# Kernel optimization log

Hardware: AMD Instinct MI355X
Metric: run time of the kernel (lower is better)

Reference implementation:

```python
import jax, jax.numpy as jnp
import numpy as np

B, PAST, FUT, D = 128, 256, 128, 128
RU, LD, FC, TL = 512, 128, 512, 128
HDEC = RU + LD  # 640


def _u(k, shape, s):
    return jax.random.uniform(k, shape, jnp.float32, -s, s)


def setup_inputs() -> dict:
    key = jax.random.key(0)
    ks = jax.random.split(key, 40)
    s_ru = 1.0 / np.sqrt(RU)
    s_hd = 1.0 / np.sqrt(HDEC)
    inp = {
        "past": jax.random.normal(ks[0], (B, PAST, D), jnp.float32),
        "future": jax.random.normal(ks[1], (B, FUT, D), jnp.float32),
        "eps": jax.random.normal(ks[2], (B, LD), jnp.float32),
        # encoder GRU over past (rnn_phi)
        "phi_Wih": _u(ks[3], (3 * RU, D), s_ru), "phi_Whh": _u(ks[4], (3 * RU, RU), s_ru),
        "phi_bih": _u(ks[5], (3 * RU,), s_ru), "phi_bhh": _u(ks[6], (3 * RU,), s_ru),
        # encoder GRU over future (rnn_x)
        "xr_Wih": _u(ks[7], (3 * RU, D), s_ru), "xr_Whh": _u(ks[8], (3 * RU, RU), s_ru),
        "xr_bih": _u(ks[9], (3 * RU,), s_ru), "xr_bhh": _u(ks[10], (3 * RU,), s_ru),
        # encoder_mu MLP: 2*RU -> 512 -> 256 -> LD
        "mu_W1": _u(ks[11], (512, 2 * RU), 1 / np.sqrt(2 * RU)), "mu_b1": _u(ks[12], (512,), 1 / np.sqrt(2 * RU)),
        "mu_W2": _u(ks[13], (256, 512), 1 / np.sqrt(512)), "mu_b2": _u(ks[14], (256,), 1 / np.sqrt(512)),
        "mu_W3": _u(ks[15], (LD, 256), 1 / np.sqrt(256)), "mu_b3": _u(ks[16], (LD,), 1 / np.sqrt(256)),
        # encoder_logvar MLP
        "lv_W1": _u(ks[17], (512, 2 * RU), 1 / np.sqrt(2 * RU)), "lv_b1": _u(ks[18], (512,), 1 / np.sqrt(2 * RU)),
        "lv_W2": _u(ks[19], (256, 512), 1 / np.sqrt(512)), "lv_b2": _u(ks[20], (256,), 1 / np.sqrt(512)),
        "lv_W3": _u(ks[21], (LD, 256), 1 / np.sqrt(256)), "lv_b3": _u(ks[22], (LD,), 1 / np.sqrt(256)),
        # decoder GRU: input D -> hidden HDEC
        "dec_Wih": _u(ks[23], (3 * HDEC, D), s_hd), "dec_Whh": _u(ks[24], (3 * HDEC, HDEC), s_hd),
        "dec_bih": _u(ks[25], (3 * HDEC,), s_hd), "dec_bhh": _u(ks[26], (3 * HDEC,), s_hd),
        # decoder heads
        "fc_W": _u(ks[27], (FC, HDEC), s_hd), "fc_b": _u(ks[28], (FC,), s_hd),
        "out_W": _u(ks[29], (D, FC), 1 / np.sqrt(FC)), "out_b": _u(ks[30], (D,), 1 / np.sqrt(FC)),
    }
    return inp


def _gru_cell(x, h, Wih, Whh, bih, bhh):
    # torch GRU cell math
    gi = x @ Wih.T + bih
    gh = h @ Whh.T + bhh
    ir, iz, inn = jnp.split(gi, 3, axis=-1)
    hr, hz, hn = jnp.split(gh, 3, axis=-1)
    r = jax.nn.sigmoid(ir + hr)
    z = jax.nn.sigmoid(iz + hz)
    n = jnp.tanh(inn + r * hn)
    return (1.0 - z) * n + z * h


def _gru_final_hidden(x, Wih, Whh, bih, bhh):
    # x: [B, T, D] -> final hidden [B, H]
    h0 = jnp.zeros((x.shape[0], Whh.shape[1]), x.dtype)
    def step(h, xt):
        h = _gru_cell(xt, h, Wih, Whh, bih, bhh)
        return h, None
    hT, _ = jax.lax.scan(step, h0, jnp.swapaxes(x, 0, 1))
    return hT


def _mlp(f, W1, b1, W2, b2, W3, b3):
    h = jax.nn.leaky_relu(f @ W1.T + b1)
    h = jax.nn.leaky_relu(h @ W2.T + b2)
    return h @ W3.T + b3


def _forward(past, future, eps,
             phi_Wih, phi_Whh, phi_bih, phi_bhh,
             xr_Wih, xr_Whh, xr_bih, xr_bhh,
             mu_W1, mu_b1, mu_W2, mu_b2, mu_W3, mu_b3,
             lv_W1, lv_b1, lv_W2, lv_b2, lv_W3, lv_b3,
             dec_Wih, dec_Whh, dec_bih, dec_bhh,
             fc_W, fc_b, out_W, out_b):
    # encoder
    h_past = _gru_final_hidden(past, phi_Wih, phi_Whh, phi_bih, phi_bhh)      # [B, RU]
    h_future = _gru_final_hidden(future, xr_Wih, xr_Whh, xr_bih, xr_bhh)      # [B, RU]
    features = jnp.concatenate([h_past, h_future], axis=1)                    # [B, 2*RU]
    z_mu = _mlp(features, mu_W1, mu_b1, mu_W2, mu_b2, mu_W3, mu_b3)
    z_logvar = _mlp(features, lv_W1, lv_b1, lv_W2, lv_b2, lv_W3, lv_b3)
    # reparameterize
    z = z_mu + eps * jnp.exp(0.5 * z_logvar)                                  # [B, LD]
    dec_h0 = jnp.concatenate([h_past, z], axis=1)                             # [B, HDEC]
    x0 = past[:, -1, :]                                                       # [B, D]
    def step(carry, _):
        x_in, h = carry
        h = _gru_cell(x_in, h, dec_Wih, dec_Whh, dec_bih, dec_bhh)
        out = jax.nn.relu(h @ fc_W.T + fc_b) @ out_W.T + out_b                # [B, D]
        return (out, h), out
    _, outs = jax.lax.scan(step, (x0, dec_h0), None, length=TL)               # [TL, B, D]
    x_mu = jnp.swapaxes(outs, 0, 1)                                           # [B, TL, D]
    return x_mu, z_mu, z_logvar


def reference(past, future, eps,
              phi_Wih, phi_Whh, phi_bih, phi_bhh,
              xr_Wih, xr_Whh, xr_bih, xr_bhh,
              mu_W1, mu_b1, mu_W2, mu_b2, mu_W3, mu_b3,
              lv_W1, lv_b1, lv_W2, lv_b2, lv_W3, lv_b3,
              dec_Wih, dec_Whh, dec_bih, dec_bhh,
              fc_W, fc_b, out_W, out_b):
    return _forward(past, future, eps,
                    phi_Wih, phi_Whh, phi_bih, phi_bhh,
                    xr_Wih, xr_Whh, xr_bih, xr_bhh,
                    mu_W1, mu_b1, mu_W2, mu_b2, mu_W3, mu_b3,
                    lv_W1, lv_b1, lv_W2, lv_b2, lv_W3, lv_b3,
                    dec_Wih, dec_Whh, dec_bih, dec_bhh,
                    fc_W, fc_b, out_W, out_b)
```

## Files before the change

### kernel.cpp

```cpp
#include <hip/hip_runtime.h>
#include <math.h>

constexpr int B    = 128;
constexpr int PAST = 256;
constexpr int FUT  = 128;
constexpr int D    = 128;
constexpr int RU   = 512;
constexpr int LD   = 128;
constexpr int TL   = 128;
constexpr int HDEC = 640;

typedef __bf16 bf16x8 __attribute__((ext_vector_type(8)));
typedef float  f32x4  __attribute__((ext_vector_type(4)));
typedef unsigned short u16x8 __attribute__((ext_vector_type(8)));

__device__ __forceinline__ unsigned short f2bf(float f) {
    unsigned int x = __float_as_uint(f);
    x = (x + 0x7fffu + ((x >> 16) & 1u)) >> 16;
    return (unsigned short)x;
}
__device__ __forceinline__ float bf2f(unsigned short u) {
    return __uint_as_float(((unsigned int)u) << 16);
}
__device__ __forceinline__ float sigm_(float x) { return 1.f / (1.f + __expf(-x)); }
__device__ __forceinline__ float tanh_(float x) {
    float e = __expf(2.f * x);
    return 1.f - 2.f / (e + 1.f);
}
__device__ __forceinline__ bf16x8 ldsfrag(const unsigned short* p) {
    return *reinterpret_cast<const bf16x8*>(p);
}
__device__ __forceinline__ f32x4 mfma16(bf16x8 a, bf16x8 b, f32x4 c) {
    return __builtin_amdgcn_mfma_f32_16x16x32_bf16(a, b, c, 0, 0, 0);
}

__global__ __launch_bounds__(256) void split_plain(
    const float* __restrict__ W, unsigned short* __restrict__ hi,
    unsigned short* __restrict__ lo, int n)
{
    for (int i = blockIdx.x * 256 + threadIdx.x; i < n; i += gridDim.x * 256) {
        float v = W[i];
        unsigned short h = f2bf(v);
        hi[i] = h;
        lo[i] = f2bf(v - bf2f(h));
    }
}

__global__ __launch_bounds__(256) void split_pack(
    const float* __restrict__ Wih, const float* __restrict__ Whh,
    int DXc, int Hc, int N3,
    unsigned short* __restrict__ hi, unsigned short* __restrict__ lo)
{
    int K = DXc + Hc;
    int total = N3 * K;
    for (int i = blockIdx.x * 256 + threadIdx.x; i < total; i += gridDim.x * 256) {
        int n = i / K, k = i - n * K;
        float v = (k < DXc) ? Wih[(size_t)n * DXc + k]
                            : Whh[(size_t)n * Hc + (k - DXc)];
        unsigned short h = f2bf(v);
        hi[i] = h;
        lo[i] = f2bf(v - bf2f(h));
    }
}

struct StepArgs {
    const float* x;  int sx;
    const float* h_in;
    const unsigned short* Whi;
    const unsigned short* Wlo;
    const float* bih; const float* bhh;
    float* h_out;
};

template<int NSET>
__device__ __forceinline__ void step_compute(
    const unsigned short* sA0, const unsigned short* sA1,
    const unsigned short* sW0, const unsigned short* sW1,
    int nlocal, int arow, int koff, f32x4 (&acc)[4][4])
{
    constexpr int LDR = 40;
    bf16x8 wh[3], wl[3];
    #pragma unroll
    for (int g = 0; g < 3; ++g) {
        wh[g] = ldsfrag(&sW0[(g * 64 + nlocal) * LDR + koff]);
        wl[g] = ldsfrag(&sW1[(g * 64 + nlocal) * LDR + koff]);
    }
    #pragma unroll
    for (int mf = 0; mf < 4; ++mf) {
        bf16x8 ah = ldsfrag(&sA0[(mf * 16 + arow) * LDR + koff]);
        bf16x8 al = ldsfrag(&sA1[(mf * 16 + arow) * LDR + koff]);
        acc[mf][0] = mfma16(ah, wh[0], acc[mf][0]);
        acc[mf][0] = mfma16(ah, wl[0], acc[mf][0]);
        acc[mf][0] = mfma16(al, wh[0], acc[mf][0]);
        acc[mf][1] = mfma16(ah, wh[1], acc[mf][1]);
        acc[mf][1] = mfma16(ah, wl[1], acc[mf][1]);
        acc[mf][1] = mfma16(al, wh[1], acc[mf][1]);
        acc[mf][NSET] = mfma16(ah, wh[2], acc[mf][NSET]);
        acc[mf][NSET] = mfma16(ah, wl[2], acc[mf][NSET]);
        acc[mf][NSET] = mfma16(al, wh[2], acc[mf][NSET]);
    }
}

template<int H, int DX>
__global__ __launch_bounds__(256, 1) void gru_step_mfma(StepArgs A0, StepArgs A1)
{
    constexpr int K   = DX + H;
    constexpr int NC  = K / 32;
    constexpr int XC  = DX / 32;
    constexpr int LDR = 40;

    __shared__ unsigned short sA[2][64 * LDR];
    __shared__ unsigned short sW[2][3 * 64 * LDR];

    const StepArgs A = (blockIdx.z == 0) ? A0 : A1;
    const int m0   = blockIdx.x * 64;
    const int hc0  = blockIdx.y * 64;
    const int tid  = threadIdx.x;
    const int lane = tid & 63;
    const int w    = tid >> 6;
    const int arow = lane & 15;
    const int koff = (lane >> 4) * 8;
    const int nlocal = w * 16 + arow;

    f32x4 acc[4][4];
    #pragma unroll
    for (int i = 0; i < 4; ++i)
        #pragma unroll
        for (int j = 0; j < 4; ++j) acc[i][j] = f32x4{0.f, 0.f, 0.f, 0.f};

    float4 ar[2];
    u16x8  wreg[6];

    auto load_chunk = [&](int c) {
        const int k0 = c * 32;
        #pragma unroll
        for (int j = 0; j < 2; ++j) {
            int id = tid + j * 256;
            int row = id >> 3, c4 = id & 7;
            const float* src = (k0 < DX)
                ? (A.x + (size_t)(m0 + row) * A.sx + (k0 + c4 * 4))
                : (A.h_in + (size_t)(m0 + row) * H + (k0 - DX + c4 * 4));
            ar[j] = *reinterpret_cast<const float4*>(src);
        }
        #pragma unroll
        for (int j = 0; j < 6; ++j) {
            int id = tid + j * 256;
            int half = (id >= 768) ? 1 : 0;
            int rem = id - half * 768;
            int gate = rem >> 8;
            int rr = (rem >> 2) & 63;
            int c8 = rem & 3;
            const unsigned short* Wp = half ? A.Wlo : A.Whi;
            wreg[j] = *reinterpret_cast<const u16x8*>(
                Wp + (size_t)(gate * H + hc0 + rr) * K + k0 + c8 * 8);
        }
    };

    auto write_chunk = [&]() {
        #pragma unroll
        for (int j = 0; j < 2; ++j) {
            int id = tid + j * 256;
            int row = id >> 3, c4 = id & 7;
            float v[4] = {ar[j].x, ar[j].y, ar[j].z, ar[j].w};
            unsigned short hs[4], ls[4];
            #pragma unroll
            for (int q = 0; q < 4; ++q) {
                hs[q] = f2bf(v[q]);
                ls[q] = f2bf(v[q] - bf2f(hs[q]));
            }
            uint2 hp, lp;
            hp.x = (unsigned)hs[0] | ((unsigned)hs[1] << 16);
            hp.y = (unsigned)hs[2] | ((unsigned)hs[3] << 16);
            lp.x = (unsigned)ls[0] | ((unsigned)ls[1] << 16);
            lp.y = (unsigned)ls[2] | ((unsigned)ls[3] << 16);
            *reinterpret_cast<uint2*>(&sA[0][row * LDR + c4 * 4]) = hp;
            *reinterpret_cast<uint2*>(&sA[1][row * LDR + c4 * 4]) = lp;
        }
        #pragma unroll
        for (int j = 0; j < 6; ++j) {
            int id = tid + j * 256;
            int half = (id >= 768) ? 1 : 0;
            int rem = id - half * 768;
            int gate = rem >> 8;
            int rr = (rem >> 2) & 63;
            int c8 = rem & 3;
            *reinterpret_cast<u16x8*>(&sW[half][(gate * 64 + rr) * LDR + c8 * 8]) = wreg[j];
        }
    };

    load_chunk(0);
    write_chunk();
    __syncthreads();
    for (int c = 0; c < NC; ++c) {
        if (c + 1 < NC) load_chunk(c + 1);
        if (c < XC) step_compute<2>(sA[0], sA[1], sW[0], sW[1], nlocal, arow, koff, acc);
        else        step_compute<3>(sA[0], sA[1], sW[0], sW[1], nlocal, arow, koff, acc);
        __syncthreads();
        if (c + 1 < NC) { write_chunk(); __syncthreads(); }
    }

    const int hc = hc0 + nlocal;
    const float bir = A.bih[hc],         bhr = A.bhh[hc];
    const float biz = A.bih[H + hc],     bhz = A.bhh[H + hc];
    const float bin = A.bih[2 * H + hc], bhn = A.bhh[2 * H + hc];
    #pragma unroll
    for (int mf = 0; mf < 4; ++mf) {
        #pragma unroll
        for (int r = 0; r < 4; ++r) {
            int m = m0 + mf * 16 + (lane >> 4) * 4 + r;
            float rg = sigm_(acc[mf][0][r] + bir + bhr);
            float zg = sigm_(acc[mf][1][r] + biz + bhz);
            float ng = tanh_((acc[mf][2][r] + bin) + rg * (acc[mf][3][r] + bhn));
            float ho = A.h_in[(size_t)m * H + hc];
            A.h_out[(size_t)m * H + hc] = (1.f - zg) * ng + zg * ho;
        }
    }
}

__global__ __launch_bounds__(256, 1) void gemm_mfma(
    const float* __restrict__ A, int lda,
    const unsigned short* __restrict__ Whi, const unsigned short* __restrict__ Wlo,
    int K, const float* __restrict__ bias,
    float* __restrict__ C, int ldc, int act)
{
    constexpr int LDR = 72;
    __shared__ unsigned short sA[2][64 * LDR];
    __shared__ unsigned short sW[2][128 * LDR];

    const int m0 = blockIdx.x * 64;
    const int n0 = blockIdx.y * 128;
    const int tid = threadIdx.x;
    const int lane = tid & 63;
    const int w = tid >> 6;
    const int arow = lane & 15;
    const int koff = (lane >> 4) * 8;

    f32x4 acc[4][2];
    #pragma unroll
    for (int i = 0; i < 4; ++i) { acc[i][0] = f32x4{0,0,0,0}; acc[i][1] = f32x4{0,0,0,0}; }

    float4 ar[4];
    u16x8  wreg[8];
    const int NC = K / 64;

    auto load_chunk = [&](int c) {
        const int k0 = c * 64;
        #pragma unroll
        for (int j = 0; j < 4; ++j) {
            int id = tid + j * 256;
            int row = id >> 4, c4 = id & 15;
            ar[j] = *reinterpret_cast<const float4*>(A + (size_t)(m0 + row) * lda + k0 + c4 * 4);
        }
        #pragma unroll
        for (int j = 0; j < 8; ++j) {
            int id = tid + j * 256;
            int half = id >> 10;
            int rem = id & 1023;
            int row = rem >> 3, c8 = rem & 7;
            const unsigned short* Wp = half ? Wlo : Whi;
            wreg[j] = *reinterpret_cast<const u16x8*>(
                Wp + (size_t)(n0 + row) * K + k0 + c8 * 8);
        }
    };
    auto write_chunk = [&]() {
        #pragma unroll
        for (int j = 0; j < 4; ++j) {
            int id = tid + j * 256;
            int row = id >> 4, c4 = id & 15;
            float v[4] = {ar[j].x, ar[j].y, ar[j].z, ar[j].w};
            unsigned short hs[4], ls[4];
            #pragma unroll
            for (int q = 0; q < 4; ++q) {
                hs[q] = f2bf(v[q]);
                ls[q] = f2bf(v[q] - bf2f(hs[q]));
            }
            uint2 hp, lp;
            hp.x = (unsigned)hs[0] | ((unsigned)hs[1] << 16);
            hp.y = (unsigned)hs[2] | ((unsigned)hs[3] << 16);
            lp.x = (unsigned)ls[0] | ((unsigned)ls[1] << 16);
            lp.y = (unsigned)ls[2] | ((unsigned)ls[3] << 16);
            *reinterpret_cast<uint2*>(&sA[0][row * LDR + c4 * 4]) = hp;
            *reinterpret_cast<uint2*>(&sA[1][row * LDR + c4 * 4]) = lp;
        }
        #pragma unroll
        for (int j = 0; j < 8; ++j) {
            int id = tid + j * 256;
            int half = id >> 10;
            int rem = id & 1023;
            int row = rem >> 3, c8 = rem & 7;
            *reinterpret_cast<u16x8*>(&sW[half][row * LDR + c8 * 8]) = wreg[j];
        }
    };

    load_chunk(0);
    write_chunk();
    __syncthreads();
    for (int c = 0; c < NC; ++c) {
        if (c + 1 < NC) load_chunk(c + 1);
        #pragma unroll
        for (int ks = 0; ks < 2; ++ks) {
            bf16x8 wh[2], wl[2];
            #pragma unroll
            for (int nf = 0; nf < 2; ++nf) {
                wh[nf] = ldsfrag(&sW[0][(w * 32 + nf * 16 + arow) * LDR + ks * 32 + koff]);
                wl[nf] = ldsfrag(&sW[1][(w * 32 + nf * 16 + arow) * LDR + ks * 32 + koff]);
            }
            #pragma unroll
            for (int mf = 0; mf < 4; ++mf) {
                bf16x8 ah = ldsfrag(&sA[0][(mf * 16 + arow) * LDR + ks * 32 + koff]);
                bf16x8 al = ldsfrag(&sA[1][(mf * 16 + arow) * LDR + ks * 32 + koff]);
                #pragma unroll
                for (int nf = 0; nf < 2; ++nf) {
                    acc[mf][nf] = mfma16(ah, wh[nf], acc[mf][nf]);
                    acc[mf][nf] = mfma16(ah, wl[nf], acc[mf][nf]);
                    acc[mf][nf] = mfma16(al, wh[nf], acc[mf][nf]);
                }
            }
        }
        __syncthreads();
        if (c + 1 < NC) { write_chunk(); __syncthreads(); }
    }

    #pragma unroll
    for (int mf = 0; mf < 4; ++mf) {
        #pragma unroll
        for (int nf = 0; nf < 2; ++nf) {
            int n = n0 + w * 32 + nf * 16 + arow;
            float bv = bias[n];
            #pragma unroll
            for (int r = 0; r < 4; ++r) {
                int m = m0 + mf * 16 + (lane >> 4) * 4 + r;
                float v = acc[mf][nf][r] + bv;
                if (act == 1)      v = (v > 0.f) ? v : 0.01f * v;
                else if (act == 2) v = fmaxf(v, 0.f);
                C[(size_t)m * ldc + n] = v;
            }
        }
    }
}

__global__ __launch_bounds__(256) void concat2(
    const float* __restrict__ A, int ka,
    const float* __restrict__ Bp, int kb,
    float* __restrict__ Y, int M)
{
    int wdt = ka + kb;
    int idx = blockIdx.x * 256 + threadIdx.x;
    if (idx >= M * wdt) return;
    int m = idx / wdt, c = idx - m * wdt;
    Y[idx] = (c < ka) ? A[(size_t)m * ka + c] : Bp[(size_t)m * kb + (c - ka)];
}

__global__ __launch_bounds__(256) void reparam(
    const float* __restrict__ zmu, const float* __restrict__ zlv,
    const float* __restrict__ eps, float* __restrict__ z, int n)
{
    int i = blockIdx.x * 256 + threadIdx.x;
    if (i < n) z[i] = zmu[i] + eps[i] * __expf(0.5f * zlv[i]);
}

extern "C" void kernel_launch(void* const* d_in, const int* in_sizes, int n_in,
                              void* d_out, int out_size, void* d_ws, size_t ws_size,
                              hipStream_t stream)
{
    const float* past    = (const float*)d_in[0];
    const float* future  = (const float*)d_in[1];
    const float* eps     = (const float*)d_in[2];
    const float* phi_Wih = (const float*)d_in[3];
    const float* phi_Whh = (const float*)d_in[4];
    const float* phi_bih = (const float*)d_in[5];
    const float* phi_bhh = (const float*)d_in[6];
    const float* xr_Wih  = (const float*)d_in[7];
    const float* xr_Whh  = (const float*)d_in[8];
    const float* xr_bih  = (const float*)d_in[9];
    const float* xr_bhh  = (const float*)d_in[10];
    const float* mu_W1   = (const float*)d_in[11];
    const float* mu_b1   = (const float*)d_in[12];
    const float* mu_W2   = (const float*)d_in[13];
    const float* mu_b2   = (const float*)d_in[14];
    const float* mu_W3   = (const float*)d_in[15];
    const float* mu_b3   = (const float*)d_in[16];
    const float* lv_W1   = (const float*)d_in[17];
    const float* lv_b1   = (const float*)d_in[18];
    const float* lv_W2   = (const float*)d_in[19];
    const float* lv_b2   = (const float*)d_in[20];
    const float* lv_W3   = (const float*)d_in[21];
    const float* lv_b3   = (const float*)d_in[22];
    const float* dec_Wih = (const float*)d_in[23];
    const float* dec_Whh = (const float*)d_in[24];
    const float* dec_bih = (const float*)d_in[25];
    const float* dec_bhh = (const float*)d_in[26];
    const float* fc_W    = (const float*)d_in[27];
    const float* fc_b    = (const float*)d_in[28];
    const float* out_W   = (const float*)d_in[29];
    const float* out_b   = (const float*)d_in[30];
    (void)in_sizes; (void)n_in; (void)out_size; (void)ws_size;

    float* out = (float*)d_out;
    float* xmu = out;
    float* zmu = out + (size_t)B * TL * D;
    float* zlv = zmu + (size_t)B * LD;

    char* p = (char*)d_ws;
    auto aus = [&](size_t n) { unsigned short* r = (unsigned short*)p; p += ((n * 2 + 255) / 256) * 256; return r; };
    auto af  = [&](size_t n) { float* r = (float*)p; p += ((n * 4 + 255) / 256) * 256; return r; };

    unsigned short* phiWhi = aus((size_t)3 * RU * (D + RU));
    unsigned short* phiWlo = aus((size_t)3 * RU * (D + RU));
    unsigned short* xrWhi  = aus((size_t)3 * RU * (D + RU));
    unsigned short* xrWlo  = aus((size_t)3 * RU * (D + RU));
    unsigned short* decWhi = aus((size_t)3 * HDEC * (D + HDEC));
    unsigned short* decWlo = aus((size_t)3 * HDEC * (D + HDEC));
    unsigned short* mW1hi = aus(512 * 1024), *mW1lo = aus(512 * 1024);
    unsigned short* mW2hi = aus(256 * 512),  *mW2lo = aus(256 * 512);
    unsigned short* mW3hi = aus(128 * 256),  *mW3lo = aus(128 * 256);
    unsigned short* lW1hi = aus(512 * 1024), *lW1lo = aus(512 * 1024);
    unsigned short* lW2hi = aus(256 * 512),  *lW2lo = aus(256 * 512);
    unsigned short* lW3hi = aus(128 * 256),  *lW3lo = aus(128 * 256);
    unsigned short* fcWhi = aus(512 * 640),  *fcWlo = aus(512 * 640);
    unsigned short* oWhi  = aus(128 * 512),  *oWlo  = aus(128 * 512);

    float* hA  = af((size_t)B * RU);
    float* hB  = af((size_t)B * RU);
    float* hxA = af((size_t)B * RU);
    float* hxB = af((size_t)B * RU);
    float* dA  = af((size_t)B * HDEC);
    float* dB  = af((size_t)B * HDEC);
    float* feat= af((size_t)B * 2 * RU);
    float* m1  = af((size_t)B * 512);
    float* m2  = af((size_t)B * 256);
    float* zb  = af((size_t)B * LD);
    float* fcb = af((size_t)B * 512);

    dim3 blk(256);

    split_pack<<<512, blk, 0, stream>>>(phi_Wih, phi_Whh, D, RU, 3 * RU, phiWhi, phiWlo);
    split_pack<<<512, blk, 0, stream>>>(xr_Wih,  xr_Whh,  D, RU, 3 * RU, xrWhi,  xrWlo);
    split_pack<<<512, blk, 0, stream>>>(dec_Wih, dec_Whh, D, HDEC, 3 * HDEC, decWhi, decWlo);
    split_plain<<<512, blk, 0, stream>>>(mu_W1, mW1hi, mW1lo, 512 * 1024);
    split_plain<<<256, blk, 0, stream>>>(mu_W2, mW2hi, mW2lo, 256 * 512);
    split_plain<<<128, blk, 0, stream>>>(mu_W3, mW3hi, mW3lo, 128 * 256);
    split_plain<<<512, blk, 0, stream>>>(lv_W1, lW1hi, lW1lo, 512 * 1024);
    split_plain<<<256, blk, 0, stream>>>(lv_W2, lW2hi, lW2lo, 256 * 512);
    split_plain<<<128, blk, 0, stream>>>(lv_W3, lW3hi, lW3lo, 128 * 256);
    split_plain<<<512, blk, 0, stream>>>(fc_W, fcWhi, fcWlo, 512 * 640);
    split_plain<<<128, blk, 0, stream>>>(out_W, oWhi, oWlo, 128 * 512);

    hipMemsetAsync(hA,  0, (size_t)B * RU * sizeof(float), stream);
    hipMemsetAsync(hxA, 0, (size_t)B * RU * sizeof(float), stream);

    for (int t = 0; t < PAST; ++t) {
        const float* phin  = (t & 1) ? hB : hA;
        float*       phout = (t & 1) ? hA : hB;
        StepArgs pa{past + (size_t)t * D, PAST * D, phin, phiWhi, phiWlo, phi_bih, phi_bhh, phout};
        if (t < FUT) {
            const float* xin  = (t & 1) ? hxB : hxA;
            float*       xout = (t & 1) ? hxA : hxB;
            StepArgs xa{future + (size_t)t * D, FUT * D, xin, xrWhi, xrWlo, xr_bih, xr_bhh, xout};
            gru_step_mfma<RU, D><<<dim3(2, RU / 64, 2), blk, 0, stream>>>(pa, xa);
        } else {
            gru_step_mfma<RU, D><<<dim3(2, RU / 64, 1), blk, 0, stream>>>(pa, pa);
        }
    }

    concat2<<<dim3((B * 2 * RU + 255) / 256), blk, 0, stream>>>(hA, RU, hxA, RU, feat, B);

    gemm_mfma<<<dim3(2, 4), blk, 0, stream>>>(feat, 2 * RU, mW1hi, mW1lo, 1024, mu_b1, m1, 512, 1);
    gemm_mfma<<<dim3(2, 2), blk, 0, stream>>>(m1, 512, mW2hi, mW2lo, 512, mu_b2, m2, 256, 1);
    gemm_mfma<<<dim3(2, 1), blk, 0, stream>>>(m2, 256, mW3hi, mW3lo, 256, mu_b3, zmu, LD, 0);
    gemm_mfma<<<dim3(2, 4), blk, 0, stream>>>(feat, 2 * RU, lW1hi, lW1lo, 1024, lv_b1, m1, 512, 1);
    gemm_mfma<<<dim3(2, 2), blk, 0, stream>>>(m1, 512, lW2hi, lW2lo, 512, lv_b2, m2, 256, 1);
    gemm_mfma<<<dim3(2, 1), blk, 0, stream>>>(m2, 256, lW3hi, lW3lo, 256, lv_b3, zlv, LD, 0);

    reparam<<<dim3((B * LD + 255) / 256), blk, 0, stream>>>(zmu, zlv, eps, zb, B * LD);
    concat2<<<dim3((B * HDEC + 255) / 256), blk, 0, stream>>>(hA, RU, zb, LD, dA, B);

    for (int t = 0; t < TL; ++t) {
        const float* xin; int sx;
        if (t == 0) { xin = past + (size_t)(PAST - 1) * D; sx = PAST * D; }
        else        { xin = xmu + (size_t)(t - 1) * D;     sx = TL * D; }
        const float* hin  = (t & 1) ? dB : dA;
        float*       hout = (t & 1) ? dA : dB;
        StepArgs da{xin, sx, hin, decWhi, decWlo, dec_bih, dec_bhh, hout};
        gru_step_mfma<HDEC, D><<<dim3(2, HDEC / 64, 1), blk, 0, stream>>>(da, da);
        gemm_mfma<<<dim3(2, 4), blk, 0, stream>>>(hout, HDEC, fcWhi, fcWlo, HDEC, fc_b, fcb, 512, 2);
        gemm_mfma<<<dim3(2, 1), blk, 0, stream>>>(fcb, 512, oWhi, oWlo, 512, out_b, xmu + (size_t)t * D, TL * D, 0);
    }
}
```

Measured before the change: 15.03 ms.

## Replace per-timestep GRU launches with persistent kernels using grid barriers

The encoder and decoder recurrences now each run as one persistent kernel rather than one launch per timestep. Workgroups keep their slice of the hi-part bf16 weights resident in LDS across all timesteps and synchronise between steps with an atomic-counter grid barrier. In the decoder, the GRU, the fc layer and the output layer run as roles inside the same kernel, separated by barriers. This removes hundreds of launch gaps and repeated weight reloads. In exchange it relies on every workgroup being co-resident (128 or 80 WGs), which is not guaranteed, and the spin barriers add latency on every step.

```diff
diff --git a/kernel.cpp b/kernel.cpp
--- a/kernel.cpp
+++ b/kernel.cpp
@@ -32,6 +32,28 @@
 }
 __device__ __forceinline__ f32x4 mfma16(bf16x8 a, bf16x8 b, f32x4 c) {
     return __builtin_amdgcn_mfma_f32_16x16x32_bf16(a, b, c, 0, 0, 0);
+}
+__device__ __forceinline__ void cvt4(const float4& v, uint2& hp, uint2& lp) {
+    float a[4] = {v.x, v.y, v.z, v.w};
+    unsigned short hs[4], ls[4];
+    #pragma unroll
+    for (int q = 0; q < 4; ++q) { hs[q] = f2bf(a[q]); ls[q] = f2bf(a[q] - bf2f(hs[q])); }
+    hp.x = (unsigned)hs[0] | ((unsigned)hs[1] << 16);
+    hp.y = (unsigned)hs[2] | ((unsigned)hs[3] << 16);
+    lp.x = (unsigned)ls[0] | ((unsigned)ls[1] << 16);
+    lp.y = (unsigned)ls[2] | ((unsigned)ls[3] << 16);
+}
+
+__device__ __forceinline__ void coop_barrier(unsigned* cnt, unsigned nwg, unsigned rnd) {
+    __syncthreads();
+    __threadfence();
+    if (threadIdx.x == 0) {
+        __hip_atomic_fetch_add(cnt, 1u, __ATOMIC_RELEASE, __HIP_MEMORY_SCOPE_AGENT);
+        unsigned tgt = (rnd + 1u) * nwg;
+        while (__hip_atomic_load(cnt, __ATOMIC_ACQUIRE, __HIP_MEMORY_SCOPE_AGENT) < tgt)
+            __builtin_amdgcn_s_sleep(2);
+    }
+    __syncthreads();
 }
 
 __global__ __launch_bounds__(256) void split_plain(
@@ -63,157 +85,364 @@
     }
 }
 
-struct StepArgs {
-    const float* x;  int sx;
-    const float* h_in;
-    const unsigned short* Whi;
-    const unsigned short* Wlo;
+struct EncArgs {
+    const float* x; int xstride; int T;
+    const unsigned short* Whi; const unsigned short* Wlo;
     const float* bih; const float* bhh;
-    float* h_out;
+    float* h0; float* h1;
+    unsigned* bar;
 };
 
-template<int NSET>
-__device__ __forceinline__ void step_compute(
-    const unsigned short* sA0, const unsigned short* sA1,
-    const unsigned short* sW0, const unsigned short* sW1,
-    int nlocal, int arow, int koff, f32x4 (&acc)[4][4])
-{
-    constexpr int LDR = 40;
-    bf16x8 wh[3], wl[3];
-    #pragma unroll
-    for (int g = 0; g < 3; ++g) {
-        wh[g] = ldsfrag(&sW0[(g * 64 + nlocal) * LDR + koff]);
-        wl[g] = ldsfrag(&sW1[(g * 64 + nlocal) * LDR + koff]);
-    }
-    #pragma unroll
-    for (int mf = 0; mf < 4; ++mf) {
-        bf16x8 ah = ldsfrag(&sA0[(mf * 16 + arow) * LDR + koff]);
-        bf16x8 al = ldsfrag(&sA1[(mf * 16 + arow) * LDR + koff]);
-        acc[mf][0] = mfma16(ah, wh[0], acc[mf][0]);
-        acc[mf][0] = mfma16(ah, wl[0], acc[mf][0]);
-        acc[mf][0] = mfma16(al, wh[0], acc[mf][0]);
-        acc[mf][1] = mfma16(ah, wh[1], acc[mf][1]);
-        acc[mf][1] = mfma16(ah, wl[1], acc[mf][1]);
-        acc[mf][1] = mfma16(al, wh[1], acc[mf][1]);
-        acc[mf][NSET] = mfma16(ah, wh[2], acc[mf][NSET]);
-        acc[mf][NSET] = mfma16(ah, wl[2], acc[mf][NSET]);
-        acc[mf][NSET] = mfma16(al, wh[2], acc[mf][NSET]);
-    }
-}
-
-template<int H, int DX>
-__global__ __launch_bounds__(256, 1) void gru_step_mfma(StepArgs A0, StepArgs A1)
-{
-    constexpr int K   = DX + H;
-    constexpr int NC  = K / 32;
-    constexpr int XC  = DX / 32;
-    constexpr int LDR = 40;
-
-    __shared__ unsigned short sA[2][64 * LDR];
-    __shared__ unsigned short sW[2][3 * 64 * LDR];
-
-    const StepArgs A = (blockIdx.z == 0) ? A0 : A1;
-    const int m0   = blockIdx.x * 64;
-    const int hc0  = blockIdx.y * 64;
-    const int tid  = threadIdx.x;
+__global__ __launch_bounds__(256, 1) void enc_kernel(EncArgs P, EncArgs X)
+{
+    constexpr int H = 512, DX = 128, K = 640, NCH = 20, XC = 4, LDK = 648, SR = 40;
+    __shared__ unsigned short sWhi[48 * LDK];
+    __shared__ unsigned short sAh[2][64 * SR];
+    __shared__ unsigned short sAl[2][64 * SR];
+    __shared__ unsigned short sWl[2][48 * SR];
+
+    const int wg = blockIdx.x;
+    const EncArgs A = (wg < 64) ? P : X;
+    const int lwg = wg & 63;
+    const int m0  = (lwg & 1) * 64;
+    const int c0  = (lwg >> 1) * 16;
+    const int tid = threadIdx.x;
     const int lane = tid & 63;
-    const int w    = tid >> 6;
+    const int w = tid >> 6;
     const int arow = lane & 15;
     const int koff = (lane >> 4) * 8;
-    const int nlocal = w * 16 + arow;
-
-    f32x4 acc[4][4];
+
+    for (int i = tid; i < 48 * 80; i += 256) {
+        int rr = i / 80, c8 = i % 80;
+        int g = rr >> 4, j = rr & 15;
+        *reinterpret_cast<u16x8*>(&sWhi[rr * LDK + c8 * 8]) =
+            *reinterpret_cast<const u16x8*>(A.Whi + (size_t)(g * H + c0 + j) * K + c8 * 8);
+    }
+    const unsigned short* wloB = nullptr;
+    if (tid < 192) {
+        int rr = tid >> 2, c8 = tid & 3;
+        int g = rr >> 4, j = rr & 15;
+        wloB = A.Wlo + (size_t)(g * H + c0 + j) * K + c8 * 8;
+    }
+    const int hc = c0 + arow;
+    const float brz0 = A.bih[hc] + A.bhh[hc];
+    const float brz1 = A.bih[H + hc] + A.bhh[H + hc];
+    const float bn_i = A.bih[2 * H + hc];
+    const float bn_h = A.bhh[2 * H + hc];
+    __syncthreads();
+
+    float4 ar[2]; u16x8 wl;
+
+    for (int t = 0; t < A.T; ++t) {
+        const float* hin  = (t & 1) ? A.h1 : A.h0;
+        float*       hout = (t & 1) ? A.h0 : A.h1;
+        const float* xp = A.x + (size_t)t * D;
+
+        f32x4 accR = {0,0,0,0}, accZ = {0,0,0,0}, accNx = {0,0,0,0}, accNh = {0,0,0,0};
+
+        auto ldc = [&](int c) {
+            int k0 = c * 32;
+            #pragma unroll
+            for (int j = 0; j < 2; ++j) {
+                int id = tid + j * 256;
+                int row = id >> 3, c4 = id & 7;
+                const float* src = (k0 < DX)
+                    ? (xp + (size_t)(m0 + row) * A.xstride + k0 + c4 * 4)
+                    : (hin + (size_t)(m0 + row) * H + (k0 - DX) + c4 * 4);
+                ar[j] = *reinterpret_cast<const float4*>(src);
+            }
+            if (wloB) wl = *reinterpret_cast<const u16x8*>(wloB + k0);
+        };
+        auto wrc = [&](int b) {
+            #pragma unroll
+            for (int j = 0; j < 2; ++j) {
+                int id = tid + j * 256;
+                int row = id >> 3, c4 = id & 7;
+                uint2 hp, lp; cvt4(ar[j], hp, lp);
+                *reinterpret_cast<uint2*>(&sAh[b][row * SR + c4 * 4]) = hp;
+                *reinterpret_cast<uint2*>(&sAl[b][row * SR + c4 * 4]) = lp;
+            }
+            if (wloB) {
+                int rr = tid >> 2, c8 = tid & 3;
+                *reinterpret_cast<u16x8*>(&sWl[b][rr * SR + c8 * 8]) = wl;
+            }
+        };
+
+        ldc(0); wrc(0); __syncthreads();
+        for (int c = 0; c < NCH; ++c) {
+            const int b = c & 1;
+            if (c + 1 < NCH) ldc(c + 1);
+            const int aoff = (w * 16 + arow) * SR + koff;
+            bf16x8 ah = ldsfrag(&sAh[b][aoff]);
+            bf16x8 al = ldsfrag(&sAl[b][aoff]);
+            bf16x8 whR = ldsfrag(&sWhi[(arow) * LDK + c * 32 + koff]);
+            bf16x8 whZ = ldsfrag(&sWhi[(16 + arow) * LDK + c * 32 + koff]);
+            bf16x8 whN = ldsfrag(&sWhi[(32 + arow) * LDK + c * 32 + koff]);
+            bf16x8 wlR = ldsfrag(&sWl[b][(arow) * SR + koff]);
+            bf16x8 wlZ = ldsfrag(&sWl[b][(16 + arow) * SR + koff]);
+            bf16x8 wlN = ldsfrag(&sWl[b][(32 + arow) * SR + koff]);
+            accR = mfma16(ah, whR, accR); accR = mfma16(ah, wlR, accR); accR = mfma16(al, whR, accR);
+            accZ = mfma16(ah, whZ, accZ); accZ = mfma16(ah, wlZ, accZ); accZ = mfma16(al, whZ, accZ);
+            if (c < XC) {
+                accNx = mfma16(ah, whN, accNx); accNx = mfma16(ah, wlN, accNx); accNx = mfma16(al, whN, accNx);
+            } else {
+                accNh = mfma16(ah, whN, accNh); accNh = mfma16(ah, wlN, accNh); accNh = mfma16(al, whN, accNh);
+            }
+            if (c + 1 < NCH) wrc(b ^ 1);
+            __syncthreads();
+        }
+
+        #pragma unroll
+        for (int r = 0; r < 4; ++r) {
+            int m = m0 + w * 16 + (lane >> 4) * 4 + r;
+            float rg = sigm_(accR[r] + brz0);
+            float zg = sigm_(accZ[r] + brz1);
+            float ng = tanh_((accNx[r] + bn_i) + rg * (accNh[r] + bn_h));
+            float ho = hin[(size_t)m * H + hc];
+            hout[(size_t)m * H + hc] = (1.f - zg) * ng + zg * ho;
+        }
+        coop_barrier(A.bar, 64, (unsigned)t);
+    }
+}
+
+struct DecArgs {
+    const float* past_last;
+    float* xmu;
+    const unsigned short* Whi; const unsigned short* Wlo;
+    const float* bih; const float* bhh;
+    const unsigned short* fcWhi; const unsigned short* fcWlo;
+    const float* fc_b;
+    const unsigned short* oWhi; const unsigned short* oWlo;
+    const float* out_b;
+    float* dh0; float* dh1; float* fcb;
+    unsigned* bar;
+};
+
+__device__ __forceinline__ void plain16(
+    unsigned short* smem, int whi_ush, int ldk, int nch,
+    const float* src, int srcld,
+    const unsigned short* wloB,
+    float bias_v, int mode,
+    float* dst, long dld, int dcol0,
+    int tid, int w, int lane, int arow, int koff)
+{
+    unsigned short* AH[2] = { smem + whi_ush,          smem + whi_ush + 5120 };
+    unsigned short* AL[2] = { smem + whi_ush + 10240,  smem + whi_ush + 15360 };
+    unsigned short* WL[2] = { smem + whi_ush + 20480,  smem + whi_ush + 21120 };
+    f32x4 acc0 = {0,0,0,0}, acc1 = {0,0,0,0};
+    float4 ar[4]; u16x8 wl;
+    auto ldc = [&](int c) {
+        int k0 = c * 32;
+        #pragma unroll
+        for (int j = 0; j < 4; ++j) {
+            int id = tid + j * 256, row = id >> 3, c4 = id & 7;
+            ar[j] = *reinterpret_cast<const float4*>(src + (size_t)row * srcld + k0 + c4 * 4);
+        }
+        if (wloB) wl = *reinterpret_cast<const u16x8*>(wloB + k0);
+    };
+    auto wrc = [&](int b) {
+        #pragma unroll
+        for (int j = 0; j < 4; ++j) {
+            int id = tid + j * 256, row = id >> 3, c4 = id & 7;
+            uint2 hp, lp; cvt4(ar[j], hp, lp);
+            *reinterpret_cast<uint2*>(&AH[b][row * 40 + c4 * 4]) = hp;
+            *reinterpret_cast<uint2*>(&AL[b][row * 40 + c4 * 4]) = lp;
+        }
+        if (wloB) {
+            int rr = tid >> 2, c8 = tid & 3;
+            *reinterpret_cast<u16x8*>(&WL[b][rr * 40 + c8 * 8]) = wl;
+        }
+    };
+    ldc(0); wrc(0); __syncthreads();
+    for (int c = 0; c < nch; ++c) {
+        int b = c & 1;
+        if (c + 1 < nch) ldc(c + 1);
+        int a0 = (w * 32 + arow) * 40 + koff;
+        bf16x8 ah0 = ldsfrag(&AH[b][a0]),       al0 = ldsfrag(&AL[b][a0]);
+        bf16x8 ah1 = ldsfrag(&AH[b][a0 + 640]), al1 = ldsfrag(&AL[b][a0 + 640]);
+        bf16x8 wh  = ldsfrag(&smem[arow * ldk + c * 32 + koff]);
+        bf16x8 wlg = ldsfrag(&WL[b][arow * 40 + koff]);
+        acc0 = mfma16(ah0, wh, acc0); acc0 = mfma16(ah0, wlg, acc0); acc0 = mfma16(al0, wh, acc0);
+        acc1 = mfma16(ah1, wh, acc1); acc1 = mfma16(ah1, wlg, acc1); acc1 = mfma16(al1, wh, acc1);
+        if (c + 1 < nch) wrc(b ^ 1);
+        __syncthreads();
+    }
     #pragma unroll
-    for (int i = 0; i < 4; ++i)
-        #pragma unroll
-        for (int j = 0; j < 4; ++j) acc[i][j] = f32x4{0.f, 0.f, 0.f, 0.f};
-
-    float4 ar[2];
-    u16x8  wreg[6];
-
-    auto load_chunk = [&](int c) {
-        const int k0 = c * 32;
-        #pragma unroll
-        for (int j = 0; j < 2; ++j) {
-            int id = tid + j * 256;
-            int row = id >> 3, c4 = id & 7;
-            const float* src = (k0 < DX)
-                ? (A.x + (size_t)(m0 + row) * A.sx + (k0 + c4 * 4))
-                : (A.h_in + (size_t)(m0 + row) * H + (k0 - DX + c4 * 4));
-            ar[j] = *reinterpret_cast<const float4*>(src);
-        }
-        #pragma unroll
-        for (int j = 0; j < 6; ++j) {
-            int id = tid + j * 256;
-            int half = (id >= 768) ? 1 : 0;
-            int rem = id - half * 768;
-            int gate = rem >> 8;
-            int rr = (rem >> 2) & 63;
-            int c8 = rem & 3;
-            const unsigned short* Wp = half ? A.Wlo : A.Whi;
-            wreg[j] = *reinterpret_cast<const u16x8*>(
-                Wp + (size_t)(gate * H + hc0 + rr) * K + k0 + c8 * 8);
-        }
+    for (int mf = 0; mf < 2; ++mf) {
+        f32x4 a = mf ? acc1 : acc0;
+        #pragma unroll
+        for (int r = 0; r < 4; ++r) {
+            int m = w * 32 + mf * 16 + (lane >> 4) * 4 + r;
+            float v = a[r] + bias_v;
+            if (mode == 1) v = fmaxf(v, 0.f);
+            dst[(size_t)m * dld + dcol0 + arow] = v;
+        }
+    }
+}
+
+__device__ __forceinline__ void dec_gru(
+    unsigned short* smem, const DecArgs& A, int t,
+    const float* hcur, float* hnext,
+    int c0, const unsigned short* wloB,
+    float brz0, float brz1, float bn_i, float bn_h,
+    int tid, int w, int lane, int arow, int koff)
+{
+    unsigned short* AH[2] = { smem + 37248, smem + 42368 };
+    unsigned short* AL[2] = { smem + 47488, smem + 52608 };
+    unsigned short* WL[2] = { smem + 57728, smem + 59648 };
+    const float* xp; long xs;
+    if (t == 0) { xp = A.past_last; xs = (long)PAST * D; }
+    else        { xp = A.xmu + (size_t)(t - 1) * D; xs = (long)TL * D; }
+
+    f32x4 aR0 = {0,0,0,0}, aZ0 = aR0, aNx0 = aR0, aNh0 = aR0;
+    f32x4 aR1 = aR0, aZ1 = aR0, aNx1 = aR0, aNh1 = aR0;
+    float4 ar[4]; u16x8 wl;
+    auto ldc = [&](int c) {
+        int k0 = c * 32;
+        #pragma unroll
+        for (int j = 0; j < 4; ++j) {
+            int id = tid + j * 256, row = id >> 3, c4 = id & 7;
+            const float* s = (k0 < D)
+                ? (xp + (size_t)row * xs + k0 + c4 * 4)
+                : (hcur + (size_t)row * HDEC + (k0 - D) + c4 * 4);
+            ar[j] = *reinterpret_cast<const float4*>(s);
+        }
+        if (wloB) wl = *reinterpret_cast<const u16x8*>(wloB + k0);
     };
-
-    auto write_chunk = [&]() {
-        #pragma unroll
-        for (int j = 0; j < 2; ++j) {
-            int id = tid + j * 256;
-            int row = id >> 3, c4 = id & 7;
-            float v[4] = {ar[j].x, ar[j].y, ar[j].z, ar[j].w};
-            unsigned short hs[4], ls[4];
-            #pragma unroll
-            for (int q = 0; q < 4; ++q) {
-                hs[q] = f2bf(v[q]);
-                ls[q] = f2bf(v[q] - bf2f(hs[q]));
-            }
-            uint2 hp, lp;
-            hp.x = (unsigned)hs[0] | ((unsigned)hs[1] << 16);
-            hp.y = (unsigned)hs[2] | ((unsigned)hs[3] << 16);
-            lp.x = (unsigned)ls[0] | ((unsigned)ls[1] << 16);
-            lp.y = (unsigned)ls[2] | ((unsigned)ls[3] << 16);
-            *reinterpret_cast<uint2*>(&sA[0][row * LDR + c4 * 4]) = hp;
-            *reinterpret_cast<uint2*>(&sA[1][row * LDR + c4 * 4]) = lp;
-        }
-        #pragma unroll
-        for (int j = 0; j < 6; ++j) {
-            int id = tid + j * 256;
-            int half = (id >= 768) ? 1 : 0;
-            int rem = id - half * 768;
-            int gate = rem >> 8;
-            int rr = (rem >> 2) & 63;
-            int c8 = rem & 3;
-            *reinterpret_cast<u16x8*>(&sW[half][(gate * 64 + rr) * LDR + c8 * 8]) = wreg[j];
+    auto wrc = [&](int b) {
+        #pragma unroll
+        for (int j = 0; j < 4; ++j) {
+            int id = tid + j * 256, row = id >> 3, c4 = id & 7;
+            uint2 hp, lp; cvt4(ar[j], hp, lp);
+            *reinterpret_cast<uint2*>(&AH[b][row * 40 + c4 * 4]) = hp;
+            *reinterpret_cast<uint2*>(&AL[b][row * 40 + c4 * 4]) = lp;
+        }
+        if (wloB) {
+            int rr = tid >> 2, c8 = tid & 3;
+            *reinterpret_cast<u16x8*>(&WL[b][rr * 40 + c8 * 8]) = wl;
         }
     };
-
-    load_chunk(0);
-    write_chunk();
+    ldc(0); wrc(0); __syncthreads();
+    for (int c = 0; c < 24; ++c) {
+        int b = c & 1;
+        if (c + 1 < 24) ldc(c + 1);
+        int a0 = (w * 32 + arow) * 40 + koff;
+        bf16x8 ah0 = ldsfrag(&AH[b][a0]),       al0 = ldsfrag(&AL[b][a0]);
+        bf16x8 ah1 = ldsfrag(&AH[b][a0 + 640]), al1 = ldsfrag(&AL[b][a0 + 640]);
+        bf16x8 whR = ldsfrag(&smem[(arow) * 776 + c * 32 + koff]);
+        bf16x8 whZ = ldsfrag(&smem[(16 + arow) * 776 + c * 32 + koff]);
+        bf16x8 whN = ldsfrag(&smem[(32 + arow) * 776 + c * 32 + koff]);
+        bf16x8 wlR = ldsfrag(&WL[b][(arow) * 40 + koff]);
+        bf16x8 wlZ = ldsfrag(&WL[b][(16 + arow) * 40 + koff]);
+        bf16x8 wlN = ldsfrag(&WL[b][(32 + arow) * 40 + koff]);
+        aR0 = mfma16(ah0, whR, aR0); aR0 = mfma16(ah0, wlR, aR0); aR0 = mfma16(al0, whR, aR0);
+        aR1 = mfma16(ah1, whR, aR1); aR1 = mfma16(ah1, wlR, aR1); aR1 = mfma16(al1, whR, aR1);
+        aZ0 = mfma16(ah0, whZ, aZ0); aZ0 = mfma16(ah0, wlZ, aZ0); aZ0 = mfma16(al0, whZ, aZ0);
+        aZ1 = mfma16(ah1, whZ, aZ1); aZ1 = mfma16(ah1, wlZ, aZ1); aZ1 = mfma16(al1, whZ, aZ1);
+        if (c < 4) {
+            aNx0 = mfma16(ah0, whN, aNx0); aNx0 = mfma16(ah0, wlN, aNx0); aNx0 = mfma16(al0, whN, aNx0);
+            aNx1 = mfma16(ah1, whN, aNx1); aNx1 = mfma16(ah1, wlN, aNx1); aNx1 = mfma16(al1, whN, aNx1);
+        } else {
+            aNh0 = mfma16(ah0, whN, aNh0); aNh0 = mfma16(ah0, wlN, aNh0); aNh0 = mfma16(al0, whN, aNh0);
+            aNh1 = mfma16(ah1, whN, aNh1); aNh1 = mfma16(ah1, wlN, aNh1); aNh1 = mfma16(al1, whN, aNh1);
+        }
+        if (c + 1 < 24) wrc(b ^ 1);
+        __syncthreads();
+    }
+    const int hcc = c0 + arow;
+    #pragma unroll
+    for (int mf = 0; mf < 2; ++mf) {
+        #pragma unroll
+        for (int r = 0; r < 4; ++r) {
+            int m = w * 32 + mf * 16 + (lane >> 4) * 4 + r;
+            float vr = mf ? aR1[r] : aR0[r];
+            float vz = mf ? aZ1[r] : aZ0[r];
+            float vx = mf ? aNx1[r] : aNx0[r];
+            float vh = mf ? aNh1[r] : aNh0[r];
+            float rg = sigm_(vr + brz0);
+            float zg = sigm_(vz + brz1);
+            float ng = tanh_((vx + bn_i) + rg * (vh + bn_h));
+            float ho = hcur[(size_t)m * HDEC + hcc];
+            hnext[(size_t)m * HDEC + hcc] = (1.f - zg) * ng + zg * ho;
+        }
+    }
+}
+
+__global__ __launch_bounds__(256, 1) void dec_kernel(DecArgs A)
+{
+    __shared__ unsigned short smem[61568];
+    const int wg = blockIdx.x;
+    const int tid = threadIdx.x;
+    const int lane = tid & 63;
+    const int w = tid >> 6;
+    const int arow = lane & 15;
+    const int koff = (lane >> 4) * 8;
+    const int role = (wg < 40) ? 0 : ((wg < 72) ? 1 : 2);
+
+    const unsigned short* wloB = nullptr;
+    float b0 = 0, b1 = 0, b2 = 0, b3 = 0;
+    int c0 = 0;
+
+    if (role == 0) {
+        c0 = wg * 16;
+        for (int i = tid; i < 4608; i += 256) {
+            int rr = i / 96, c8 = i % 96;
+            int g = rr >> 4, j = rr & 15;
+            *reinterpret_cast<u16x8*>(&smem[rr * 776 + c8 * 8]) =
+                *reinterpret_cast<const u16x8*>(A.Whi + (size_t)(g * HDEC + c0 + j) * 768 + c8 * 8);
+        }
+        if (tid < 192) {
+            int rr = tid >> 2, c8 = tid & 3;
+            int g = rr >> 4, j = rr & 15;
+            wloB = A.Wlo + (size_t)(g * HDEC + c0 + j) * 768 + c8 * 8;
+        }
+        int hcc = c0 + arow;
+        b0 = A.bih[hcc] + A.bhh[hcc];
+        b1 = A.bih[HDEC + hcc] + A.bhh[HDEC + hcc];
+        b2 = A.bih[2 * HDEC + hcc];
+        b3 = A.bhh[2 * HDEC + hcc];
+    } else if (role == 1) {
+        c0 = (wg - 40) * 16;
+        for (int i = tid; i < 1280; i += 256) {
+            int rr = i / 80, c8 = i % 80;
+            *reinterpret_cast<u16x8*>(&smem[rr * 648 + c8 * 8]) =
+                *reinterpret_cast<const u16x8*>(A.fcWhi + (size_t)(c0 + rr) * 640 + c8 * 8);
+        }
+        if (tid < 64) {
+            int rr = tid >> 2, c8 = tid & 3;
+            wloB = A.fcWlo + (size_t)(c0 + rr) * 640 + c8 * 8;
+        }
+        b0 = A.fc_b[c0 + arow];
+    } else {
+        c0 = (wg - 72) * 16;
+        for (int i = tid; i < 1024; i += 256) {
+            int rr = i >> 6, c8 = i & 63;
+            *reinterpret_cast<u16x8*>(&smem[rr * 520 + c8 * 8]) =
+                *reinterpret_cast<const u16x8*>(A.oWhi + (size_t)(c0 + rr) * 512 + c8 * 8);
+        }
+        if (tid < 64) {
+            int rr = tid >> 2, c8 = tid & 3;
+            wloB = A.oWlo + (size_t)(c0 + rr) * 512 + c8 * 8;
+        }
+        b0 = A.out_b[c0 + arow];
+    }
     __syncthreads();
-    for (int c = 0; c < NC; ++c) {
-        if (c + 1 < NC) load_chunk(c + 1);
-        if (c < XC) step_compute<2>(sA[0], sA[1], sW[0], sW[1], nlocal, arow, koff, acc);
-        else        step_compute<3>(sA[0], sA[1], sW[0], sW[1], nlocal, arow, koff, acc);
-        __syncthreads();
-        if (c + 1 < NC) { write_chunk(); __syncthreads(); }
-    }
-
-    const int hc = hc0 + nlocal;
-    const float bir = A.bih[hc],         bhr = A.bhh[hc];
-    const float biz = A.bih[H + hc],     bhz = A.bhh[H + hc];
-    const float bin = A.bih[2 * H + hc], bhn = A.bhh[2 * H + hc];
-    #pragma unroll
-    for (int mf = 0; mf < 4; ++mf) {
-        #pragma unroll
-        for (int r = 0; r < 4; ++r) {
-            int m = m0 + mf * 16 + (lane >> 4) * 4 + r;
-            float rg = sigm_(acc[mf][0][r] + bir + bhr);
-            float zg = sigm_(acc[mf][1][r] + biz + bhz);
-            float ng = tanh_((acc[mf][2][r] + bin) + rg * (acc[mf][3][r] + bhn));
-            float ho = A.h_in[(size_t)m * H + hc];
-            A.h_out[(size_t)m * H + hc] = (1.f - zg) * ng + zg * ho;
-        }
+
+    unsigned rnd = 0;
+    for (int t = 0; t < TL; ++t) {
+        const float* hcur = (t & 1) ? A.dh1 : A.dh0;
+        float*       hnext = (t & 1) ? A.dh0 : A.dh1;
+        if (role == 0)
+            dec_gru(smem, A, t, hcur, hnext, c0, wloB, b0, b1, b2, b3, tid, w, lane, arow, koff);
+        coop_barrier(A.bar, 80, rnd++);
+        if (role == 1)
+            plain16(smem, 10368, 648, 20, hnext, HDEC, wloB, b0, 1, A.fcb, 512, c0,
+                    tid, w, lane, arow, koff);
+        coop_barrier(A.bar, 80, rnd++);
+        if (role == 2)
+            plain16(smem, 8320, 520, 16, A.fcb, 512, wloB, b0, 0,
+                    A.xmu + (size_t)t * D, (long)TL * D, c0, tid, w, lane, arow, koff);
+        coop_barrier(A.bar, 80, rnd++);
     }
 }
 
@@ -258,8 +487,7 @@
             int rem = id & 1023;
             int row = rem >> 3, c8 = rem & 7;
             const unsigned short* Wp = half ? Wlo : Whi;
-            wreg[j] = *reinterpret_cast<const u16x8*>(
-                Wp + (size_t)(n0 + row) * K + k0 + c8 * 8);
+            wreg[j] = *reinterpret_cast<const u16x8*>(Wp + (size_t)(n0 + row) * K + k0 + c8 * 8);
         }
     };
     auto write_chunk = [&]() {
@@ -267,18 +495,7 @@
         for (int j = 0; j < 4; ++j) {
             int id = tid + j * 256;
             int row = id >> 4, c4 = id & 15;
-            float v[4] = {ar[j].x, ar[j].y, ar[j].z, ar[j].w};
-            unsigned short hs[4], ls[4];
-            #pragma unroll
-            for (int q = 0; q < 4; ++q) {
-                hs[q] = f2bf(v[q]);
-                ls[q] = f2bf(v[q] - bf2f(hs[q]));
-            }
-            uint2 hp, lp;
-            hp.x = (unsigned)hs[0] | ((unsigned)hs[1] << 16);
-            hp.y = (unsigned)hs[2] | ((unsigned)hs[3] << 16);
-            lp.x = (unsigned)ls[0] | ((unsigned)ls[1] << 16);
-            lp.y = (unsigned)ls[2] | ((unsigned)ls[3] << 16);
+            uint2 hp, lp; cvt4(ar[j], hp, lp);
             *reinterpret_cast<uint2*>(&sA[0][row * LDR + c4 * 4]) = hp;
             *reinterpret_cast<uint2*>(&sA[1][row * LDR + c4 * 4]) = lp;
         }
@@ -299,11 +516,11 @@
         if (c + 1 < NC) load_chunk(c + 1);
         #pragma unroll
         for (int ks = 0; ks < 2; ++ks) {
-            bf16x8 wh[2], wl[2];
+            bf16x8 wh[2], wlv[2];
             #pragma unroll
             for (int nf = 0; nf < 2; ++nf) {
-                wh[nf] = ldsfrag(&sW[0][(w * 32 + nf * 16 + arow) * LDR + ks * 32 + koff]);
-                wl[nf] = ldsfrag(&sW[1][(w * 32 + nf * 16 + arow) * LDR + ks * 32 + koff]);
+                wh[nf]  = ldsfrag(&sW[0][(w * 32 + nf * 16 + arow) * LDR + ks * 32 + koff]);
+                wlv[nf] = ldsfrag(&sW[1][(w * 32 + nf * 16 + arow) * LDR + ks * 32 + koff]);
             }
             #pragma unroll
             for (int mf = 0; mf < 4; ++mf) {
@@ -312,7 +529,7 @@
                 #pragma unroll
                 for (int nf = 0; nf < 2; ++nf) {
                     acc[mf][nf] = mfma16(ah, wh[nf], acc[mf][nf]);
-                    acc[mf][nf] = mfma16(ah, wl[nf], acc[mf][nf]);
+                    acc[mf][nf] = mfma16(ah, wlv[nf], acc[mf][nf]);
                     acc[mf][nf] = mfma16(al, wh[nf], acc[mf][nf]);
                 }
             }
@@ -402,6 +619,7 @@
     float* zlv = zmu + (size_t)B * LD;
 
     char* p = (char*)d_ws;
+    unsigned* bars = (unsigned*)p; p += 4096;
     auto aus = [&](size_t n) { unsigned short* r = (unsigned short*)p; p += ((n * 2 + 255) / 256) * 256; return r; };
     auto af  = [&](size_t n) { float* r = (float*)p; p += ((n * 4 + 255) / 256) * 256; return r; };
 
@@ -424,8 +642,8 @@
     float* hB  = af((size_t)B * RU);
     float* hxA = af((size_t)B * RU);
     float* hxB = af((size_t)B * RU);
-    float* dA  = af((size_t)B * HDEC);
-    float* dB  = af((size_t)B * HDEC);
+    float* dh0 = af((size_t)B * HDEC);
+    float* dh1 = af((size_t)B * HDEC);
     float* feat= af((size_t)B * 2 * RU);
     float* m1  = af((size_t)B * 512);
     float* m2  = af((size_t)B * 256);
@@ -446,22 +664,13 @@
     split_plain<<<512, blk, 0, stream>>>(fc_W, fcWhi, fcWlo, 512 * 640);
     split_plain<<<128, blk, 0, stream>>>(out_W, oWhi, oWlo, 128 * 512);
 
+    hipMemsetAsync(bars, 0, 4096, stream);
     hipMemsetAsync(hA,  0, (size_t)B * RU * sizeof(float), stream);
     hipMemsetAsync(hxA, 0, (size_t)B * RU * sizeof(float), stream);
 
-    for (int t = 0; t < PAST; ++t) {
-        const float* phin  = (t & 1) ? hB : hA;
-        float*       phout = (t & 1) ? hA : hB;
-        StepArgs pa{past + (size_t)t * D, PAST * D, phin, phiWhi, phiWlo, phi_bih, phi_bhh, phout};
-        if (t < FUT) {
-            const float* xin  = (t & 1) ? hxB : hxA;
-            float*       xout = (t & 1) ? hxA : hxB;
-            StepArgs xa{future + (size_t)t * D, FUT * D, xin, xrWhi, xrWlo, xr_bih, xr_bhh, xout};
-            gru_step_mfma<RU, D><<<dim3(2, RU / 64, 2), blk, 0, stream>>>(pa, xa);
-        } else {
-            gru_step_mfma<RU, D><<<dim3(2, RU / 64, 1), blk, 0, stream>>>(pa, pa);
-        }
-    }
+    EncArgs eP{past,   PAST * D, PAST, phiWhi, phiWlo, phi_bih, phi_bhh, hA,  hB,  bars + 0};
+    EncArgs eX{future, FUT * D,  FUT,  xrWhi,  xrWlo,  xr_bih,  xr_bhh,  hxA, hxB, bars + 64};
+    enc_kernel<<<dim3(128), blk, 0, stream>>>(eP, eX);
 
     concat2<<<dim3((B * 2 * RU + 255) / 256), blk, 0, stream>>>(hA, RU, hxA, RU, feat, B);
 
@@ -473,17 +682,12 @@
     gemm_mfma<<<dim3(2, 1), blk, 0, stream>>>(m2, 256, lW3hi, lW3lo, 256, lv_b3, zlv, LD, 0);
 
     reparam<<<dim3((B * LD + 255) / 256), blk, 0, stream>>>(zmu, zlv, eps, zb, B * LD);
-    concat2<<<dim3((B * HDEC + 255) / 256), blk, 0, stream>>>(hA, RU, zb, LD, dA, B);
-
-    for (int t = 0; t < TL; ++t) {
-        const float* xin; int sx;
-        if (t == 0) { xin = past + (size_t)(PAST - 1) * D; sx = PAST * D; }
-        else        { xin = xmu + (size_t)(t - 1) * D;     sx = TL * D; }
-        const float* hin  = (t & 1) ? dB : dA;
-        float*       hout = (t & 1) ? dA : dB;
-        StepArgs da{xin, sx, hin, decWhi, decWlo, dec_bih, dec_bhh, hout};
-        gru_step_mfma<HDEC, D><<<dim3(2, HDEC / 64, 1), blk, 0, stream>>>(da, da);
-        gemm_mfma<<<dim3(2, 4), blk, 0, stream>>>(hout, HDEC, fcWhi, fcWlo, HDEC, fc_b, fcb, 512, 2);
-        gemm_mfma<<<dim3(2, 1), blk, 0, stream>>>(fcb, 512, oWhi, oWlo, 512, out_b, xmu + (size_t)t * D, TL * D, 0);
-    }
-}
+    concat2<<<dim3((B * HDEC + 255) / 256), blk, 0, stream>>>(hA, RU, zb, LD, dh0, B);
+
+    DecArgs dA_{past + (size_t)(PAST - 1) * D, xmu,
+                decWhi, decWlo, dec_bih, dec_bhh,
+                fcWhi, fcWlo, fc_b,
+                oWhi, oWlo, out_b,
+                dh0, dh1, fcb, bars + 128};
+    dec_kernel<<<dim3(80), blk, 0, stream>>>(dA_);
+}
```

Measured after the change: 17.76 ms. 18.2% more time.
